# Kernel optimization log

Measured on AMD Instinct MI355X. Metric: run time of the kernel, lower is better.

Reference implementation:

```python
import jax, jax.numpy as jnp
import numpy as np

DE_NEIGHBORS = 8

def _cdist(a, b):
    # a: [B,N,C], b: [B,S,C] -> [B,N,S] euclidean distance
    d2 = (jnp.sum(a * a, -1)[:, :, None] + jnp.sum(b * b, -1)[:, None, :]
          - 2.0 * jnp.einsum('bnc,bsc->bns', a, b))
    return jnp.sqrt(jnp.maximum(d2, 0.0))

def _propagate(xyz1, xyz2, n1, n2, p1, p2, k):
    # xyz1/n1: [B,N,3] fine; xyz2/n2: [B,S,3] coarse; p1: [B,N,C]; p2: [B,S,C]
    dists = _cdist(xyz1, xyz2) + jax.nn.sigmoid(_cdist(n1, n2))  # [B,N,S]
    negd, idx = jax.lax.top_k(-dists, k)                         # k smallest
    d = -negd
    recip = 1.0 / (d + 1e-8)
    w = recip / jnp.sum(recip, axis=-1, keepdims=True)           # [B,N,k]
    gathered = jax.vmap(lambda p, i: p[i])(p2, idx)              # [B,N,k,C]
    interp = jnp.einsum('bnkc,bnk->bnc', gathered, w)
    # cat=False merge: elementwise (max + mean)/2 of (p1, interp)
    return (jnp.maximum(p1, interp) + (p1 + interp) * 0.5) * 0.5

def setup_inputs() -> dict:
    key = jax.random.key(0)
    ks = jax.random.split(key, 12)
    Ns = [16384, 4096, 1024, 256]
    B, C = 2, 256
    out = {}
    for i, N in enumerate(Ns):
        out[f'xyz{i}'] = jax.random.normal(ks[i], (B, N, 3), jnp.float32)
        out[f'nrm{i}'] = jax.random.normal(ks[4 + i], (B, N, 3), jnp.float32)
        out[f'feat{i}'] = jax.random.normal(ks[8 + i], (B, N, C), jnp.float32)
    return out

def reference(xyz0, xyz1, xyz2, xyz3, nrm0, nrm1, nrm2, nrm3,
              feat0, feat1, feat2, feat3):
    # forward reverses the lists: index 0 = coarsest
    xyzs = [xyz3, xyz2, xyz1, xyz0]
    nrms = [nrm3, nrm2, nrm1, nrm0]
    pts = [feat3, feat2, feat1, feat0]
    x = pts[0]
    for i in range(3):  # num_stages
        x = _propagate(xyzs[i + 1], xyzs[i], nrms[i + 1], nrms[i],
                       pts[i + 1], x, DE_NEIGHBORS)
    return x
```

## Files before the change

kernel.cpp:

```cpp
#include <hip/hip_runtime.h>

#define KNBR 8

__global__ __launch_bounds__(256) void pack_kernel(
    const float* __restrict__ xa, const float* __restrict__ na, int ca,
    const float* __restrict__ xb, const float* __restrict__ nb, int cb,
    const float* __restrict__ xc, const float* __restrict__ nc_, int cc,
    float* __restrict__ pa, float* __restrict__ pb, float* __restrict__ pc)
{
#pragma clang fp contract(off)
    int t = blockIdx.x * blockDim.x + threadIdx.x;
    const float* xs; const float* ns; float* dst; int i;
    if (t < ca)            { xs = xa; ns = na;  dst = pa; i = t; }
    else if (t < ca + cb)  { xs = xb; ns = nb;  dst = pb; i = t - ca; }
    else if (t < ca+cb+cc) { xs = xc; ns = nc_; dst = pc; i = t - ca - cb; }
    else return;
    float x = xs[3*i], y = xs[3*i+1], z = xs[3*i+2];
    float u = ns[3*i], v = ns[3*i+1], w = ns[3*i+2];
    float4 r0 = make_float4(x, y, z, (x*x + y*y) + z*z);
    float4 r1 = make_float4(u, v, w, (u*u + v*v) + w*w);
    reinterpret_cast<float4*>(dst)[2*i]     = r0;
    reinterpret_cast<float4*>(dst)[2*i + 1] = r1;
}

#define CEX(V, I, A, B) { bool sw_ = V[B] < V[A];                       \
    float lo_ = sw_ ? V[B] : V[A]; float hi_ = sw_ ? V[A] : V[B];       \
    int   li_ = sw_ ? I[B] : I[A]; int   hj_ = sw_ ? I[A] : I[B];       \
    V[A] = lo_; V[B] = hi_; I[A] = li_; I[B] = hj_; }

template<int L>
__global__ __launch_bounds__(256) void topk_kernel(
    const float* __restrict__ xyzF, const float* __restrict__ nrmF,
    const float* __restrict__ packC, int NF, int NC,
    int* __restrict__ outIdx, float* __restrict__ outW)
{
    const int lane = threadIdx.x & (L - 1);
    const int grp  = (blockIdx.x * blockDim.x + threadIdx.x) / L;
    const int b    = grp >= NF ? 1 : 0;

    const float* fp = xyzF + (size_t)grp * 3;
    float fx = fp[0], fy = fp[1], fz = fp[2];
    const float* gp = nrmF + (size_t)grp * 3;
    float gx = gp[0], gy = gp[1], gz = gp[2];
    float sax = fmaf(fx, fx, fmaf(fy, fy, fz * fz));
    float san = fmaf(gx, gx, fmaf(gy, gy, gz * gz));

    float d[KNBR]; int id[KNBR];
#pragma unroll
    for (int j = 0; j < KNBR; ++j) { d[j] = 3.402823466e38f; id[j] = 0; }

    const float4* base = reinterpret_cast<const float4*>(packC) + (size_t)b * NC * 2;
    const int nch = NC / (8 * L);
    for (int cc = 0; cc < nch; ++cc) {
        const int s0 = cc * (8 * L) + lane;
        const float4* p = base + (size_t)s0 * 2;
        float4 q0[8], q1[8];
#pragma unroll
        for (int k = 0; k < 8; ++k) { q0[k] = p[2*L*k]; q1[k] = p[2*L*k + 1]; }

        float cv[8]; int ci[8];
#pragma unroll
        for (int k = 0; k < 8; ++k) {
            float dot = fmaf(fx, q0[k].x, fmaf(fy, q0[k].y, fz * q0[k].z));
            float d2  = fmaf(-2.0f, dot, sax + q0[k].w);
            float dxx = __builtin_amdgcn_sqrtf(fmaxf(d2, 0.0f));
            float dtn = fmaf(gx, q1[k].x, fmaf(gy, q1[k].y, gz * q1[k].z));
            float d2n = fmaf(-2.0f, dtn, san + q1[k].w);
            float dnn = __builtin_amdgcn_sqrtf(fmaxf(d2n, 0.0f));
            float sg  = __builtin_amdgcn_rcpf(1.0f + __expf(-dnn));
            cv[k] = dxx + sg;
            ci[k] = s0 + k * L;
        }

        CEX(cv,ci,0,1) CEX(cv,ci,2,3) CEX(cv,ci,4,5) CEX(cv,ci,6,7)
        CEX(cv,ci,0,2) CEX(cv,ci,1,3) CEX(cv,ci,4,6) CEX(cv,ci,5,7)
        CEX(cv,ci,1,2) CEX(cv,ci,5,6)
        CEX(cv,ci,0,4) CEX(cv,ci,1,5) CEX(cv,ci,2,6) CEX(cv,ci,3,7)
        CEX(cv,ci,2,4) CEX(cv,ci,3,5)
        CEX(cv,ci,1,2) CEX(cv,ci,3,4) CEX(cv,ci,5,6)

        float nd[KNBR]; int ni[KNBR];
#pragma unroll
        for (int i = 0; i < KNBR; ++i) {
            bool t = cv[KNBR-1-i] < d[i];
            nd[i] = t ? cv[KNBR-1-i] : d[i];
            ni[i] = t ? ci[KNBR-1-i] : id[i];
        }
        CEX(nd,ni,0,4) CEX(nd,ni,1,5) CEX(nd,ni,2,6) CEX(nd,ni,3,7)
        CEX(nd,ni,0,2) CEX(nd,ni,1,3) CEX(nd,ni,4,6) CEX(nd,ni,5,7)
        CEX(nd,ni,0,1) CEX(nd,ni,2,3) CEX(nd,ni,4,5) CEX(nd,ni,6,7)
#pragma unroll
        for (int j = 0; j < KNBR; ++j) { d[j] = nd[j]; id[j] = ni[j]; }
    }

#pragma unroll
    for (int m = 1; m < L; m <<= 1) {
        float pd[KNBR]; int pi[KNBR];
#pragma unroll
        for (int j = 0; j < KNBR; ++j) {
            pd[j] = __shfl_xor(d[j], m);
            pi[j] = __shfl_xor(id[j], m);
        }
        float nd[KNBR]; int ni[KNBR];
#pragma unroll
        for (int j = 0; j < KNBR; ++j) {
            bool t = pd[KNBR-1-j] < d[j];
            nd[j] = t ? pd[KNBR-1-j] : d[j];
            ni[j] = t ? pi[KNBR-1-j] : id[j];
        }
        CEX(nd,ni,0,4) CEX(nd,ni,1,5) CEX(nd,ni,2,6) CEX(nd,ni,3,7)
        CEX(nd,ni,0,2) CEX(nd,ni,1,3) CEX(nd,ni,4,6) CEX(nd,ni,5,7)
        CEX(nd,ni,0,1) CEX(nd,ni,2,3) CEX(nd,ni,4,5) CEX(nd,ni,6,7)
#pragma unroll
        for (int j = 0; j < KNBR; ++j) { d[j] = nd[j]; id[j] = ni[j]; }
    }

    if (lane == 0) {
        float r[KNBR]; float sum = 0.f;
#pragma unroll
        for (int j = 0; j < KNBR; ++j) { r[j] = 1.0f / (d[j] + 1e-8f); sum += r[j]; }
        int*   oi = outIdx + (size_t)grp * KNBR;
        float* ow = outW   + (size_t)grp * KNBR;
#pragma unroll
        for (int j = 0; j < KNBR; ++j) { oi[j] = id[j]; ow[j] = r[j] / sum; }
    }
}

__global__ __launch_bounds__(256) void interp_kernel(
    const float* __restrict__ p1, const float* __restrict__ p2,
    const int* __restrict__ idx, const float* __restrict__ w,
    int NF, int NC, float* __restrict__ out)
{
    const int pt = blockIdx.x * 4 + (threadIdx.x >> 6);
    const int c4 = threadIdx.x & 63;
    const int b  = pt >= NF ? 1 : 0;
    const int*   ip = idx + (size_t)pt * KNBR;
    const float* wp = w   + (size_t)pt * KNBR;
    const float4* p2b = reinterpret_cast<const float4*>(p2) + (size_t)b * NC * 64;
    float4 acc = make_float4(0.f, 0.f, 0.f, 0.f);
#pragma unroll
    for (int j = 0; j < KNBR; ++j) {
        int   ii = ip[j];
        float ww = wp[j];
        float4 r = p2b[(size_t)ii * 64 + c4];
        acc.x += ww * r.x; acc.y += ww * r.y;
        acc.z += ww * r.z; acc.w += ww * r.w;
    }
    float4 a = reinterpret_cast<const float4*>(p1)[(size_t)pt * 64 + c4];
    float4 o;
    o.x = (fmaxf(a.x, acc.x) + (a.x + acc.x) * 0.5f) * 0.5f;
    o.y = (fmaxf(a.y, acc.y) + (a.y + acc.y) * 0.5f) * 0.5f;
    o.z = (fmaxf(a.z, acc.z) + (a.z + acc.z) * 0.5f) * 0.5f;
    o.w = (fmaxf(a.w, acc.w) + (a.w + acc.w) * 0.5f) * 0.5f;
    reinterpret_cast<float4*>(out)[(size_t)pt * 64 + c4] = o;
}

extern "C" void kernel_launch(void* const* d_in, const int* in_sizes, int n_in,
                              void* d_out, int out_size, void* d_ws, size_t ws_size,
                              hipStream_t stream)
{
    const float* xyz0  = (const float*)d_in[0];
    const float* nrm0  = (const float*)d_in[1];
    const float* feat0 = (const float*)d_in[2];
    const float* xyz1  = (const float*)d_in[3];
    const float* nrm1  = (const float*)d_in[4];
    const float* feat1 = (const float*)d_in[5];
    const float* xyz2  = (const float*)d_in[6];
    const float* nrm2  = (const float*)d_in[7];
    const float* feat2 = (const float*)d_in[8];
    const float* xyz3  = (const float*)d_in[9];
    const float* nrm3  = (const float*)d_in[10];
    const float* feat3 = (const float*)d_in[11];

    const int B = 2, C = 256;
    const int N0 = 16384, N1 = 4096, N2 = 1024, N3 = 256;

    float* ws = (float*)d_ws;
    size_t off = 0;
    float* pack1 = ws + off; off += (size_t)B*N1*8;
    float* pack2 = ws + off; off += (size_t)B*N2*8;
    float* pack3 = ws + off; off += (size_t)B*N3*8;
    int*   idx0  = (int*)(ws + off); off += (size_t)B*N2*KNBR;
    float* w0    = ws + off;         off += (size_t)B*N2*KNBR;
    int*   idx1  = (int*)(ws + off); off += (size_t)B*N1*KNBR;
    float* w1    = ws + off;         off += (size_t)B*N1*KNBR;
    int*   idx2  = (int*)(ws + off); off += (size_t)B*N0*KNBR;
    float* w2    = ws + off;         off += (size_t)B*N0*KNBR;
    float* x0    = ws + off;         off += (size_t)B*N2*C;
    float* x1    = ws + off;         off += (size_t)B*N1*C;

    int packTot = B * (N1 + N2 + N3);
    pack_kernel<<<(packTot + 255)/256, 256, 0, stream>>>(
        xyz1, nrm1, B*N1, xyz2, nrm2, B*N2, xyz3, nrm3, B*N3,
        pack1, pack2, pack3);

    topk_kernel<8><<<(B*N0*8)/256, 256, 0, stream>>>(xyz0, nrm0, pack1, N0, N1, idx2, w2);
    topk_kernel<8><<<(B*N1*8)/256, 256, 0, stream>>>(xyz1, nrm1, pack2, N1, N2, idx1, w1);
    topk_kernel<8><<<(B*N2*8)/256, 256, 0, stream>>>(xyz2, nrm2, pack3, N2, N3, idx0, w0);

    interp_kernel<<<(B*N2)/4, 256, 0, stream>>>(feat2, feat3, idx0, w0, N2, N3, x0);
    interp_kernel<<<(B*N1)/4, 256, 0, stream>>>(feat1, x0,    idx1, w1, N1, N2, x1);
    interp_kernel<<<(B*N0)/4, 256, 0, stream>>>(feat0, x1,    idx2, w2, N0, N1, (float*)d_out);
}
```

Before: 344.0 us.

## Fuse three top-k launches into one grid and widen lane groups to 16

Merges the three per-stage top-k kernels into a single launch whose blocks are partitioned by block index across the three stages. Each query point now uses 16 lanes instead of 8, which doubles the number of threads and cuts each lane's serial scan over the coarse points. The -2 factor is folded into the packed coarse coordinates so each distance needs one fewer multiply. The trade-off is more shuffle-merge rounds per point and a small change in rounding order that could reorder near-tied neighbors.

```diff
diff --git a/kernel.cpp b/kernel.cpp
--- a/kernel.cpp
+++ b/kernel.cpp
@@ -17,8 +17,8 @@
     else return;
     float x = xs[3*i], y = xs[3*i+1], z = xs[3*i+2];
     float u = ns[3*i], v = ns[3*i+1], w = ns[3*i+2];
-    float4 r0 = make_float4(x, y, z, (x*x + y*y) + z*z);
-    float4 r1 = make_float4(u, v, w, (u*u + v*v) + w*w);
+    float4 r0 = make_float4(-2.f*x, -2.f*y, -2.f*z, (x*x + y*y) + z*z);
+    float4 r1 = make_float4(-2.f*u, -2.f*v, -2.f*w, (u*u + v*v) + w*w);
     reinterpret_cast<float4*>(dst)[2*i]     = r0;
     reinterpret_cast<float4*>(dst)[2*i + 1] = r1;
 }
@@ -29,13 +29,13 @@
     V[A] = lo_; V[B] = hi_; I[A] = li_; I[B] = hj_; }
 
 template<int L>
-__global__ __launch_bounds__(256) void topk_kernel(
-    const float* __restrict__ xyzF, const float* __restrict__ nrmF,
+__device__ __forceinline__ void topk_body(
+    int vblk, const float* __restrict__ xyzF, const float* __restrict__ nrmF,
     const float* __restrict__ packC, int NF, int NC,
     int* __restrict__ outIdx, float* __restrict__ outW)
 {
     const int lane = threadIdx.x & (L - 1);
-    const int grp  = (blockIdx.x * blockDim.x + threadIdx.x) / L;
+    const int grp  = (vblk * 256 + (int)threadIdx.x) / L;
     const int b    = grp >= NF ? 1 : 0;
 
     const float* fp = xyzF + (size_t)grp * 3;
@@ -61,11 +61,11 @@
         float cv[8]; int ci[8];
 #pragma unroll
         for (int k = 0; k < 8; ++k) {
-            float dot = fmaf(fx, q0[k].x, fmaf(fy, q0[k].y, fz * q0[k].z));
-            float d2  = fmaf(-2.0f, dot, sax + q0[k].w);
+            float d2  = fmaf(fx, q0[k].x, fmaf(fy, q0[k].y,
+                        fmaf(fz, q0[k].z, sax + q0[k].w)));
             float dxx = __builtin_amdgcn_sqrtf(fmaxf(d2, 0.0f));
-            float dtn = fmaf(gx, q1[k].x, fmaf(gy, q1[k].y, gz * q1[k].z));
-            float d2n = fmaf(-2.0f, dtn, san + q1[k].w);
+            float d2n = fmaf(gx, q1[k].x, fmaf(gy, q1[k].y,
+                        fmaf(gz, q1[k].z, san + q1[k].w)));
             float dnn = __builtin_amdgcn_sqrtf(fmaxf(d2n, 0.0f));
             float sg  = __builtin_amdgcn_rcpf(1.0f + __expf(-dnn));
             cv[k] = dxx + sg;
@@ -124,6 +124,28 @@
 #pragma unroll
         for (int j = 0; j < KNBR; ++j) { oi[j] = id[j]; ow[j] = r[j] / sum; }
     }
+}
+
+#define G2 2048
+#define G1 512
+#define G0 128
+__global__ __launch_bounds__(256) void topk_fused(
+    const float* __restrict__ xyz0, const float* __restrict__ nrm0,
+    const float* __restrict__ xyz1, const float* __restrict__ nrm1,
+    const float* __restrict__ xyz2, const float* __restrict__ nrm2,
+    const float* __restrict__ pack1, const float* __restrict__ pack2,
+    const float* __restrict__ pack3,
+    int* __restrict__ idx2, float* __restrict__ w2,
+    int* __restrict__ idx1, float* __restrict__ w1,
+    int* __restrict__ idx0, float* __restrict__ w0)
+{
+    const int blk = blockIdx.x;
+    if (blk < G2)
+        topk_body<16>(blk, xyz0, nrm0, pack1, 16384, 4096, idx2, w2);
+    else if (blk < G2 + G1)
+        topk_body<16>(blk - G2, xyz1, nrm1, pack2, 4096, 1024, idx1, w1);
+    else
+        topk_body<16>(blk - G2 - G1, xyz2, nrm2, pack3, 1024, 256, idx0, w0);
 }
 
 __global__ __launch_bounds__(256) void interp_kernel(
@@ -194,9 +216,9 @@
         xyz1, nrm1, B*N1, xyz2, nrm2, B*N2, xyz3, nrm3, B*N3,
         pack1, pack2, pack3);
 
-    topk_kernel<8><<<(B*N0*8)/256, 256, 0, stream>>>(xyz0, nrm0, pack1, N0, N1, idx2, w2);
-    topk_kernel<8><<<(B*N1*8)/256, 256, 0, stream>>>(xyz1, nrm1, pack2, N1, N2, idx1, w1);
-    topk_kernel<8><<<(B*N2*8)/256, 256, 0, stream>>>(xyz2, nrm2, pack3, N2, N3, idx0, w0);
+    topk_fused<<<G2 + G1 + G0, 256, 0, stream>>>(
+        xyz0, nrm0, xyz1, nrm1, xyz2, nrm2,
+        pack1, pack2, pack3, idx2, w2, idx1, w1, idx0, w0);
 
     interp_kernel<<<(B*N2)/4, 256, 0, stream>>>(feat2, feat3, idx0, w0, N2, N3, x0);
     interp_kernel<<<(B*N1)/4, 256, 0, stream>>>(feat1, x0,    idx1, w1, N1, N2, x1);
```

New measurement: 291.0 us. 1.18x faster.
